# Performance work log

Measured on AMD Instinct MI355X. Metric: run time of the kernel, lower is better.

## Reference

```python
import jax, jax.numpy as jnp
import numpy as np

N, E, D = 50000, 400000, 64
L, NA, NS = 5, 4, 3            # layers, num aggregators, num scalers
ATOM_C, ATOM_V = 9, 64         # OGB-style atom feature columns / vocab
BOND_C, BOND_V = 3, 8
EPS = 1e-5
AVG_LOG = float(np.log(9.0))   # avg_d['log'] = ln(avg_degree + 1), avg_degree = 8


def setup_inputs() -> dict:
    key = jax.random.key(0)
    ks = jax.random.split(key, 8)
    x = jax.random.randint(ks[0], (N, ATOM_C), 0, ATOM_V)
    edge_index = jax.random.randint(ks[1], (2, E), 0, N)
    edge_attr = jax.random.randint(ks[2], (E, BOND_C), 0, BOND_V)
    init = lambda k, shape, fan: (jax.random.normal(k, shape, jnp.float32) / np.sqrt(fan))
    atom_emb = init(ks[3], (ATOM_C, ATOM_V, D), D)
    bond_emb = init(ks[4], (BOND_C, BOND_V, D), D)
    pre_W = init(ks[5], (L, 3 * D, D), 3 * D)                 # pretrans: Linear(3D -> D)
    pre_b = jnp.zeros((L, D), jnp.float32)
    post_W = init(ks[6], (L, (NA * NS + 1) * D, D), (NA * NS + 1) * D)  # posttrans: Linear(13D -> D)
    post_b = jnp.zeros((L, D), jnp.float32)
    return dict(x=x, edge_index=edge_index, edge_attr=edge_attr,
                atom_emb=atom_emb, bond_emb=bond_emb,
                pre_W=pre_W, pre_b=pre_b, post_W=post_W, post_b=post_b)


def reference(x, edge_index, edge_attr, atom_emb, bond_emb, pre_W, pre_b, post_W, post_b):
    src, dst = edge_index[0], edge_index[1]  # PyG: x_j = x[edge_index[0]], x_i = x[edge_index[1]]
    # Encoders: sum of per-column categorical embeddings (OGB Atom/BondEncoder)
    h0 = atom_emb[jnp.arange(ATOM_C)[None, :], x].sum(axis=1)        # [N, D]
    e = bond_emb[jnp.arange(BOND_C)[None, :], edge_attr].sum(axis=1)  # [E, D]
    # message input cat([x_i, x_j, edge_attr]) -- identical for every layer since
    # PNAGNN.forward never feeds layer output back in as x (faithful to source)
    z2 = jnp.concatenate([h0[dst], h0[src], e], axis=-1)              # [E, 3D]
    deg = jax.ops.segment_sum(jnp.ones((E,), jnp.float32), dst, num_segments=N)
    degc = jnp.maximum(deg, 1.0)[:, None]
    log_deg = jnp.log(jnp.maximum(deg, 1.0) + 1.0)[:, None]           # guard deg=0 for attenuation
    amp = log_deg / AVG_LOG
    att = AVG_LOG / log_deg
    has = (deg > 0)[:, None]
    h_in = h0
    for l in range(L):
        m = z2 @ pre_W[l] + pre_b[l]                                  # pretrans (1 layer, no act)
        s_sum = jax.ops.segment_sum(m, dst, num_segments=N)
        mean = s_sum / degc
        mx = jnp.where(has, jax.ops.segment_max(m, dst, num_segments=N), 0.0)
        mn = jnp.where(has, jax.ops.segment_min(m, dst, num_segments=N), 0.0)
        mean_sq = jax.ops.segment_sum(m * m, dst, num_segments=N) / degc
        var = jax.nn.relu(mean_sq - mean * mean)
        std = jnp.sqrt(var + EPS)
        agg = jnp.concatenate([mean, mx, mn, std], axis=-1)           # [N, 4D]
        scaled = jnp.concatenate([agg, agg * amp, agg * att], axis=-1)  # [N, 12D]
        hcat = jnp.concatenate([scaled, h0], axis=-1)                 # [N, 13D]
        out = hcat @ post_W[l] + post_b[l]                            # posttrans (1 layer, no act)
        h = out + h_in                                                # PNAGNN residual
        h_in = h
    return h
```

## Files before the change

kernel.cpp:

```cpp
#include <hip/hip_runtime.h>
#include <hip/hip_bf16.h>

#define NN 50000
#define NE 400000
#define AVG_LOG_F 2.1972245773362196f
#define EPSV 1e-5f

typedef __hip_bfloat16 bf16;
typedef __attribute__((ext_vector_type(8))) short short8v;
typedef __attribute__((ext_vector_type(4))) float f32x4;
typedef __attribute__((ext_vector_type(2))) _Float16 h2v;

__device__ __forceinline__ float b2f(bf16 v){ return __bfloat162float(v); }
__device__ __forceinline__ bf16  f2b(float v){ return __float2bfloat16(v); }
__device__ __forceinline__ short f2s(float v){
  bf16 b = __float2bfloat16(v);
  short s; __builtin_memcpy(&s, &b, 2); return s;
}
__device__ __forceinline__ float s2f(short v){
  bf16 b; __builtin_memcpy(&b, &v, 2); return __bfloat162float(b);
}

__global__ void k_h0(const int* __restrict__ x, const float* __restrict__ aemb,
                     bf16* __restrict__ h0b){
  int idx = blockIdx.x * 256 + threadIdx.x;
  if (idx >= NN * 64) return;
  int n = idx >> 6, d = idx & 63;
  float acc = 0.f;
  #pragma unroll
  for (int c = 0; c < 9; ++c){
    int a = x[n * 9 + c];
    acc += aemb[(c * 64 + a) * 64 + d];
  }
  h0b[idx] = f2b(acc);
}

__global__ void k_deg_code(const int* __restrict__ ei, const int* __restrict__ ea,
                           int* __restrict__ deg, int* __restrict__ code){
  int e = blockIdx.x * 256 + threadIdx.x;
  if (e >= NE) return;
  int dst = ei[NE + e];
  atomicAdd(&deg[dst], 1);
  code[e] = ea[e * 3] + 8 * ea[e * 3 + 1] + 64 * ea[e * 3 + 2];
}

__global__ void k_scan1(const int* __restrict__ deg, int* __restrict__ rowptr,
                        int* __restrict__ part){
  __shared__ int s[256];
  int t = threadIdx.x, i = blockIdx.x * 256 + t;
  int v = (i < NN) ? deg[i] : 0;
  s[t] = v; __syncthreads();
  for (int off = 1; off < 256; off <<= 1){
    int xv = (t >= off) ? s[t - off] : 0;
    __syncthreads();
    s[t] += xv;
    __syncthreads();
  }
  if (i < NN) rowptr[i] = s[t] - v;
  if (t == 255) part[blockIdx.x] = s[255];
}

__global__ void k_scan2(int* __restrict__ part, int nblk){
  __shared__ int s[256];
  int t = threadIdx.x;
  int v = (t < nblk) ? part[t] : 0;
  s[t] = v; __syncthreads();
  for (int off = 1; off < 256; off <<= 1){
    int xv = (t >= off) ? s[t - off] : 0;
    __syncthreads();
    s[t] += xv;
    __syncthreads();
  }
  if (t < nblk) part[t] = s[t] - v;
}

__global__ void k_scan3(int* __restrict__ rowptr, const int* __restrict__ part,
                        const int* __restrict__ deg, float* __restrict__ amp,
                        float* __restrict__ att){
  int i = blockIdx.x * 256 + threadIdx.x;
  if (i < NN){
    rowptr[i] += part[blockIdx.x];
    int d = deg[i];
    float ld = logf((float)max(d, 1) + 1.0f);
    amp[i] = ld / AVG_LOG_F;
    att[i] = AVG_LOG_F / ld;
  }
  if (i == 0) rowptr[NN] = NE;
}

__global__ void k_scatter(const int* __restrict__ ei, const int* __restrict__ code,
                          const int* __restrict__ rowptr, int* __restrict__ cursor,
                          int2* __restrict__ sedge){
  int e = blockIdx.x * 256 + threadIdx.x;
  if (e >= NE) return;
  int dst = ei[NE + e];
  int pos = rowptr[dst] + atomicAdd(&cursor[dst], 1);
  int2 v; v.x = ei[e] * 1664 + 640; v.y = code[e] * 1024;
  sedge[pos] = v;
}

__global__ void k_ctab(const float* __restrict__ bemb, const float* __restrict__ preW,
                       _Float16* __restrict__ CTp){
  __shared__ float et[64];
  int cb = blockIdx.x, l = blockIdx.y, t = threadIdx.x;
  int a0 = cb & 7, a1 = (cb >> 3) & 7, a2 = (cb >> 6) & 7;
  et[t] = bemb[(0 * 8 + a0) * 64 + t] + bemb[(1 * 8 + a1) * 64 + t] + bemb[(2 * 8 + a2) * 64 + t];
  __syncthreads();
  float acc = 0.f;
  const float* W = preW + (l * 192 + 128) * 64;
  for (int k = 0; k < 64; ++k) acc += et[k] * W[k * 64 + t];
  CTp[((size_t)cb * 64 + t) * 8 + l] = (_Float16)acc;
}

__global__ void k_whsum(const float* __restrict__ postW, const float* __restrict__ postb,
                        float* __restrict__ whs, float* __restrict__ bs){
  int idx = blockIdx.x * 256 + threadIdx.x;
  if (idx < 4096){
    int k = idx >> 6, d = idx & 63;
    float a = 0.f;
    for (int l = 0; l < 5; ++l) a += postW[(size_t)(l * 832 + 768 + k) * 64 + d];
    whs[idx] = a;
  }
  if (idx < 64){
    float a = 0.f;
    for (int l = 0; l < 5; ++l) a += postb[l * 64 + idx];
    bs[idx] = a;
  }
}

__global__ void k_wtk(const float* __restrict__ postW, bf16* __restrict__ WtKf){
  int idx = blockIdx.x * 256 + threadIdx.x;
  if (idx >= 40 * 12 * 64 * 8) return;
  int s   = idx / 6144;
  int rem = idx % 6144;
  int gw  = rem / 512;
  int lane = (rem % 512) / 8;
  int j   = idx & 7;
  int g = gw >> 2, w4 = gw & 3;
  int kp = s * 32 + (lane >> 4) * 8 + j;
  int l = kp >> 8, kl = kp & 255;
  int c = w4 * 16 + (lane & 15);
  WtKf[idx] = f2b(postW[((size_t)l * 832 + g * 256 + kl) * 64 + c]);
}

__global__ void k_wtpre896(const float* __restrict__ preW, const float* __restrict__ preb,
                           const float* __restrict__ whs, const float* __restrict__ bs,
                           bf16* __restrict__ Wtp, float* __restrict__ bias896){
  int idx = blockIdx.x * 256 + threadIdx.x;
  if (idx < 896 * 64){
    int gc = idx >> 6, k = idx & 63;
    float v;
    if (gc < 320){
      int l = gc >> 6, c = gc & 63;
      v = preW[(size_t)(l * 192 + k) * 64 + c];
    } else if (gc < 832){
      int q = gc - 320, d = q >> 3, l = q & 7;
      v = (l < 5) ? preW[(size_t)(l * 192 + 64 + k) * 64 + d] : 0.f;
    } else {
      int c = gc - 832;
      v = whs[k * 64 + c] + ((k == c) ? 1.f : 0.f);
    }
    Wtp[idx] = f2b(v);
  }
  if (idx < 896){
    float b;
    if (idx < 320)      b = preb[(idx >> 6) * 64 + (idx & 63)];
    else if (idx < 832) b = 0.f;
    else                b = bs[idx - 832];
    bias896[idx] = b;
  }
}

__global__ __launch_bounds__(256) void k_ab_mfma(const bf16* __restrict__ h0b,
                                                 const bf16* __restrict__ Wtp,
                                                 const float* __restrict__ bias896,
                                                 _Float16* __restrict__ ABU,
                                                 float* __restrict__ out){
  __shared__ bf16 As[128][72];
  __shared__ bf16 Bs[128][72];
  const int t = threadIdx.x;
  const int n0 = blockIdx.x * 128;
  const int gc0 = blockIdx.y * 128;
  const int lane = t & 63, wid = t >> 6;
  const int rw = wid * 32;
  const short* H  = (const short*)h0b;
  const short* Wp = (const short*)Wtp;

  #pragma unroll
  for (int i = 0; i < 4; ++i){
    int idx = t + i * 256;
    int r = idx >> 3, ko = (idx & 7) * 8;
    int n = n0 + r;
    short8v v = short8v{0,0,0,0,0,0,0,0};
    if (n < NN) v = *(const short8v*)(H + (size_t)n * 64 + ko);
    *(short8v*)&As[r][ko] = v;
  }
  #pragma unroll
  for (int i = 0; i < 4; ++i){
    int idx = t + i * 256;
    int cc = idx >> 3, ko = (idx & 7) * 8;
    *(short8v*)&Bs[cc][ko] = *(const short8v*)(Wp + (size_t)(gc0 + cc) * 64 + ko);
  }
  __syncthreads();

  f32x4 acc[2][8] = {};
  #pragma unroll
  for (int kk = 0; kk < 2; ++kk){
    short8v af0 = *(const short8v*)&As[rw + (lane & 15)][kk * 32 + (lane >> 4) * 8];
    short8v af1 = *(const short8v*)&As[rw + 16 + (lane & 15)][kk * 32 + (lane >> 4) * 8];
    #pragma unroll
    for (int j = 0; j < 8; ++j){
      short8v bfj = *(const short8v*)&Bs[j * 16 + (lane & 15)][kk * 32 + (lane >> 4) * 8];
      acc[0][j] = __builtin_amdgcn_mfma_f32_16x16x32_bf16(af0, bfj, acc[0][j], 0, 0, 0);
      acc[1][j] = __builtin_amdgcn_mfma_f32_16x16x32_bf16(af1, bfj, acc[1][j], 0, 0, 0);
    }
  }

  #pragma unroll
  for (int i = 0; i < 2; ++i){
    #pragma unroll
    for (int r = 0; r < 4; ++r){
      int n = n0 + rw + i * 16 + (lane >> 4) * 4 + r;
      if (n >= NN) continue;
      #pragma unroll
      for (int j = 0; j < 8; ++j){
        int gc = gc0 + j * 16 + (lane & 15);
        float v = acc[i][j][r] + bias896[gc];
        if (gc < 832) ABU[(size_t)n * 832 + gc] = (_Float16)v;
        else          out[(size_t)n * 64 + (gc - 832)] = v;
      }
    }
  }
}

__global__ __launch_bounds__(256) void k_gather(const _Float16* __restrict__ ABU,
                                                const _Float16* __restrict__ CTp,
                                                const int* __restrict__ rowptr,
                                                const int2* __restrict__ sedge,
                                                bf16* __restrict__ AGG){
  const int t = threadIdx.x, lane = t & 63, wid = t >> 6;
  const int n = blockIdx.x * 4 + wid;
  const char* ABUb = (const char*)ABU;
  const char* CTpb = (const char*)CTp;
  short* AGs = (short*)AGG;

  int r0 = rowptr[n], r1 = rowptr[n + 1];
  float s[5]  = {0.f, 0.f, 0.f, 0.f, 0.f};
  float sq[5] = {0.f, 0.f, 0.f, 0.f, 0.f};
  const _Float16 FLO = (_Float16)(-65504.f);
  const _Float16 FHI = (_Float16)( 65504.f);
  h2v mx01 = h2v{FLO, FLO}, mx23 = h2v{FLO, FLO}, mx45 = h2v{FLO, FLO};
  h2v mn01 = h2v{FHI, FHI}, mn23 = h2v{FHI, FHI}, mn45 = h2v{FHI, FHI};

  union P8 { short8v s; h2v h[4]; };
  const int lb = lane * 16;

  for (int j = r0; j < r1; j += 4){
    int rem = r1 - j;
    int2 e0 = sedge[j];
    int2 e1 = (rem > 1) ? sedge[j + 1] : e0;
    int2 e2 = (rem > 2) ? sedge[j + 2] : e0;
    int2 e3 = (rem > 3) ? sedge[j + 3] : e0;
    P8 a0, c0, a1, c1, a2, c2, a3, c3;
    a0.s = *(const short8v*)(ABUb + e0.x + lb);
    c0.s = *(const short8v*)(CTpb + e0.y + lb);
    a1.s = *(const short8v*)(ABUb + e1.x + lb);
    c1.s = *(const short8v*)(CTpb + e1.y + lb);
    a2.s = *(const short8v*)(ABUb + e2.x + lb);
    c2.s = *(const short8v*)(CTpb + e2.y + lb);
    a3.s = *(const short8v*)(ABUb + e3.x + lb);
    c3.s = *(const short8v*)(CTpb + e3.y + lb);

    #define EDGE_ACC(A, C) {                                        \
      h2v t01 = A.h[0] + C.h[0];                                    \
      h2v t23 = A.h[1] + C.h[1];                                    \
      h2v t45 = A.h[2] + C.h[2];                                    \
      mx01 = __builtin_elementwise_max(mx01, t01);                  \
      mx23 = __builtin_elementwise_max(mx23, t23);                  \
      mx45 = __builtin_elementwise_max(mx45, t45);                  \
      mn01 = __builtin_elementwise_min(mn01, t01);                  \
      mn23 = __builtin_elementwise_min(mn23, t23);                  \
      mn45 = __builtin_elementwise_min(mn45, t45);                  \
      float f0 = (float)t01[0], f1 = (float)t01[1];                 \
      float f2 = (float)t23[0], f3 = (float)t23[1];                 \
      float f4 = (float)t45[0];                                     \
      s[0] += f0; sq[0] = fmaf(f0, f0, sq[0]);                      \
      s[1] += f1; sq[1] = fmaf(f1, f1, sq[1]);                      \
      s[2] += f2; sq[2] = fmaf(f2, f2, sq[2]);                      \
      s[3] += f3; sq[3] = fmaf(f3, f3, sq[3]);                      \
      s[4] += f4; sq[4] = fmaf(f4, f4, sq[4]);                      \
    }
    EDGE_ACC(a0, c0);
    if (rem > 1) EDGE_ACC(a1, c1);
    if (rem > 2) EDGE_ACC(a2, c2);
    if (rem > 3) EDGE_ACC(a3, c3);
    #undef EDGE_ACC
  }

  float mx[5] = {(float)mx01[0], (float)mx01[1], (float)mx23[0], (float)mx23[1], (float)mx45[0]};
  float mn[5] = {(float)mn01[0], (float)mn01[1], (float)mn23[0], (float)mn23[1], (float)mn45[0]};

  int d = r1 - r0;
  float degc = (float)((d > 0) ? d : 1);
  size_t base = (size_t)n * 1280;
  #pragma unroll
  for (int l = 0; l < 5; ++l){
    float K = (float)ABU[(size_t)n * 832 + l * 64 + lane];
    float mean = ((float)d * K + s[l]) / degc;
    float MX = (d > 0) ? (K + mx[l]) : 0.f;
    float MN = (d > 0) ? (K + mn[l]) : 0.f;
    float mu = s[l] / degc;
    float var = fmaxf(sq[l] / degc - mu * mu, 0.f);
    float sd = sqrtf(var + EPSV);
    AGs[base + l * 256 + lane]       = f2s(mean);
    AGs[base + l * 256 + 64 + lane]  = f2s(MX);
    AGs[base + l * 256 + 128 + lane] = f2s(MN);
    AGs[base + l * 256 + 192 + lane] = f2s(sd);
  }
}

__global__ __launch_bounds__(256) void k_post5(const bf16* __restrict__ AGG,
                                               const bf16* __restrict__ WtKf,
                                               const float* __restrict__ amp,
                                               const float* __restrict__ att,
                                               float* __restrict__ out){
  const int t = threadIdx.x, lane = t & 63, w4 = t >> 6;
  const int rg0 = blockIdx.x * 2;
  const char* pa0 = (const char*)AGG +
      ((size_t)(rg0 * 16) + (lane & 15)) * 2560 + (lane >> 4) * 16;
  const char* pa1 = pa0 + 16 * 2560;
  const char* pb  = (const char*)WtKf + w4 * 1024 + lane * 16;

  f32x4 acc[2][3] = {};
  for (int s = 0; s < 40; ++s){
    short8v a0 = *(const short8v*)(pa0);
    short8v a1 = *(const short8v*)(pa1);
    short8v b0 = *(const short8v*)(pb);
    short8v b1 = *(const short8v*)(pb + 4096);
    short8v b2 = *(const short8v*)(pb + 8192);
    acc[0][0] = __builtin_amdgcn_mfma_f32_16x16x32_bf16(a0, b0, acc[0][0], 0, 0, 0);
    acc[0][1] = __builtin_amdgcn_mfma_f32_16x16x32_bf16(a0, b1, acc[0][1], 0, 0, 0);
    acc[0][2] = __builtin_amdgcn_mfma_f32_16x16x32_bf16(a0, b2, acc[0][2], 0, 0, 0);
    acc[1][0] = __builtin_amdgcn_mfma_f32_16x16x32_bf16(a1, b0, acc[1][0], 0, 0, 0);
    acc[1][1] = __builtin_amdgcn_mfma_f32_16x16x32_bf16(a1, b1, acc[1][1], 0, 0, 0);
    acc[1][2] = __builtin_amdgcn_mfma_f32_16x16x32_bf16(a1, b2, acc[1][2], 0, 0, 0);
    pa0 += 64; pa1 += 64; pb += 12288;
  }

  #pragma unroll
  for (int i = 0; i < 2; ++i){
    #pragma unroll
    for (int r = 0; r < 4; ++r){
      int n = (rg0 + i) * 16 + (lane >> 4) * 4 + r;
      if (n >= NN) continue;
      float am = amp[n], at = att[n];
      int c = w4 * 16 + (lane & 15);
      out[(size_t)n * 64 + c] += acc[i][0][r] + am * acc[i][1][r] + at * acc[i][2][r];
    }
  }
}

extern "C" void kernel_launch(void* const* d_in, const int* in_sizes, int n_in,
                              void* d_out, int out_size, void* d_ws, size_t ws_size,
                              hipStream_t stream){
  const int*   x     = (const int*)d_in[0];
  const int*   ei    = (const int*)d_in[1];
  const int*   ea    = (const int*)d_in[2];
  const float* aemb  = (const float*)d_in[3];
  const float* bemb  = (const float*)d_in[4];
  const float* preW  = (const float*)d_in[5];
  const float* preb  = (const float*)d_in[6];
  const float* postW = (const float*)d_in[7];
  const float* postb = (const float*)d_in[8];
  float* out = (float*)d_out;

  char* p = (char*)d_ws;
  auto alloc = [&](size_t bytes) -> char* {
    char* r = p;
    p += (bytes + 255) & ~(size_t)255;
    return r;
  };
  bf16*      h0b     = (bf16*)     alloc((size_t)NN * 64 * 2);
  _Float16*  ABU     = (_Float16*) alloc((size_t)NN * 832 * 2);
  bf16*      AGG     = (bf16*)     alloc((size_t)(NN + 16) * 1280 * 2);
  int*       deg     = (int*)      alloc((size_t)NN * 4);
  int*       rowptr  = (int*)      alloc((size_t)(NN + 1) * 4);
  int*       cursor  = (int*)      alloc((size_t)NN * 4);
  float*     amp     = (float*)    alloc((size_t)NN * 4);
  float*     att     = (float*)    alloc((size_t)NN * 4);
  int*       code    = (int*)      alloc((size_t)NE * 4);
  int2*      sedge   = (int2*)     alloc((size_t)NE * 8);
  _Float16*  CTp     = (_Float16*) alloc((size_t)512 * 64 * 8 * 2 + 64);
  float*     whs     = (float*)    alloc((size_t)64 * 64 * 4);
  float*     bs      = (float*)    alloc((size_t)64 * 4);
  int*       part    = (int*)      alloc((size_t)256 * 4);
  bf16*      WtKf    = (bf16*)     alloc((size_t)40 * 12 * 64 * 8 * 2);
  bf16*      Wtp     = (bf16*)     alloc((size_t)896 * 64 * 2);
  float*     bias896 = (float*)    alloc((size_t)896 * 4);
  if ((size_t)(p - (char*)d_ws) > ws_size) return;

  hipMemsetAsync(deg, 0, (size_t)NN * 4, stream);
  hipMemsetAsync(cursor, 0, (size_t)NN * 4, stream);

  k_h0<<<dim3((NN * 64 + 255) / 256), 256, 0, stream>>>(x, aemb, h0b);
  k_deg_code<<<dim3((NE + 255) / 256), 256, 0, stream>>>(ei, ea, deg, code);
  int nblk = (NN + 255) / 256;
  k_scan1<<<dim3(nblk), 256, 0, stream>>>(deg, rowptr, part);
  k_scan2<<<dim3(1), 256, 0, stream>>>(part, nblk);
  k_scan3<<<dim3(nblk), 256, 0, stream>>>(rowptr, part, deg, amp, att);
  k_scatter<<<dim3((NE + 255) / 256), 256, 0, stream>>>(ei, code, rowptr, cursor, sedge);
  k_ctab<<<dim3(512, 5), 64, 0, stream>>>(bemb, preW, CTp);
  k_whsum<<<dim3(16), 256, 0, stream>>>(postW, postb, whs, bs);
  k_wtk<<<dim3((40 * 12 * 64 * 8 + 255) / 256), 256, 0, stream>>>(postW, WtKf);
  k_wtpre896<<<dim3((896 * 64 + 255) / 256), 256, 0, stream>>>(preW, preb, whs, bs,
                                                               Wtp, bias896);
  k_ab_mfma<<<dim3((NN + 127) / 128, 7), 256, 0, stream>>>(h0b, Wtp, bias896, ABU, out);
  k_gather<<<dim3(NN / 4), 256, 0, stream>>>(ABU, CTp, rowptr, sedge, AGG);
  k_post5<<<dim3((3125 + 1) / 2), 256, 0, stream>>>(AGG, WtKf, amp, att, out);
}
```

Before: 310.3 us.

## Compact per-node and edge-table layouts to remove padded lanes in gather

The per-source message-part buffer and the bond-code table drop from 8 padded layer slots to 5. They are stored as a 4-wide packed chunk plus a separate 1-wide chunk, so each lane of the gather loads 8+2 bytes instead of 16 bytes per edge. The node row is reorganised to 1280 bytes, and the fifth layer's max/min is tracked in fp32. The post-GEMM loop is also manually double-buffered so the next iteration's operands load while the current MFMAs run. This cuts wasted random-gather bandwidth, at the cost of twice as many, smaller load instructions per edge.

```diff
diff --git a/kernel.cpp b/kernel.cpp
--- a/kernel.cpp
+++ b/kernel.cpp
@@ -17,8 +17,9 @@
   bf16 b = __float2bfloat16(v);
   short s; __builtin_memcpy(&s, &b, 2); return s;
 }
-__device__ __forceinline__ float s2f(short v){
-  bf16 b; __builtin_memcpy(&b, &v, 2); return __bfloat162float(b);
+__device__ __forceinline__ short f2h(float v){
+  _Float16 h = (_Float16)v;
+  short s; __builtin_memcpy(&s, &h, 2); return s;
 }
 
 __global__ void k_h0(const int* __restrict__ x, const float* __restrict__ aemb,
@@ -95,7 +96,7 @@
   if (e >= NE) return;
   int dst = ei[NE + e];
   int pos = rowptr[dst] + atomicAdd(&cursor[dst], 1);
-  int2 v; v.x = ei[e] * 1664 + 640; v.y = code[e] * 1024;
+  int2 v; v.x = ei[e] * 1280; v.y = code[e] * 640;
   sedge[pos] = v;
 }
 
@@ -109,7 +110,9 @@
   float acc = 0.f;
   const float* W = preW + (l * 192 + 128) * 64;
   for (int k = 0; k < 64; ++k) acc += et[k] * W[k * 64 + t];
-  CTp[((size_t)cb * 64 + t) * 8 + l] = (_Float16)acc;
+  char* base = (char*)CTp + (size_t)cb * 640;
+  if (l < 4) *(short*)(base + t * 8 + l * 2) = f2h(acc);
+  else       *(short*)(base + 512 + t * 2)   = f2h(acc);
 }
 
 __global__ void k_whsum(const float* __restrict__ postW, const float* __restrict__ postb,
@@ -174,7 +177,7 @@
 __global__ __launch_bounds__(256) void k_ab_mfma(const bf16* __restrict__ h0b,
                                                  const bf16* __restrict__ Wtp,
                                                  const float* __restrict__ bias896,
-                                                 _Float16* __restrict__ ABU,
+                                                 char* __restrict__ ABU,
                                                  float* __restrict__ out){
   __shared__ bf16 As[128][72];
   __shared__ bf16 Bs[128][72];
@@ -222,26 +225,36 @@
     for (int r = 0; r < 4; ++r){
       int n = n0 + rw + i * 16 + (lane >> 4) * 4 + r;
       if (n >= NN) continue;
+      char* nb = ABU + (size_t)n * 1280;
       #pragma unroll
       for (int j = 0; j < 8; ++j){
         int gc = gc0 + j * 16 + (lane & 15);
         float v = acc[i][j][r] + bias896[gc];
-        if (gc < 832) ABU[(size_t)n * 832 + gc] = (_Float16)v;
-        else          out[(size_t)n * 64 + (gc - 832)] = v;
+        if (gc < 320){
+          *(short*)(nb + gc * 2) = f2h(v);
+        } else if (gc < 832){
+          int q = gc - 320, dd = q >> 3, l = q & 7;
+          if (l < 4)       *(short*)(nb + 640 + dd * 8 + l * 2) = f2h(v);
+          else if (l == 4) *(short*)(nb + 1152 + dd * 2)        = f2h(v);
+        } else {
+          out[(size_t)n * 64 + (gc - 832)] = v;
+        }
       }
     }
   }
 }
 
-__global__ __launch_bounds__(256) void k_gather(const _Float16* __restrict__ ABU,
-                                                const _Float16* __restrict__ CTp,
+__global__ __launch_bounds__(256) void k_gather(const char* __restrict__ ABU,
+                                                const char* __restrict__ CTp,
                                                 const int* __restrict__ rowptr,
                                                 const int2* __restrict__ sedge,
                                                 bf16* __restrict__ AGG){
   const int t = threadIdx.x, lane = t & 63, wid = t >> 6;
   const int n = blockIdx.x * 4 + wid;
-  const char* ABUb = (const char*)ABU;
-  const char* CTpb = (const char*)CTp;
+  const char* AB8 = ABU + 640;
+  const char* AB2 = ABU + 1152;
+  const char* CT8 = CTp;
+  const char* CT2 = CTp + 512;
   short* AGs = (short*)AGG;
 
   int r0 = rowptr[n], r1 = rowptr[n + 1];
@@ -249,11 +262,12 @@
   float sq[5] = {0.f, 0.f, 0.f, 0.f, 0.f};
   const _Float16 FLO = (_Float16)(-65504.f);
   const _Float16 FHI = (_Float16)( 65504.f);
-  h2v mx01 = h2v{FLO, FLO}, mx23 = h2v{FLO, FLO}, mx45 = h2v{FLO, FLO};
-  h2v mn01 = h2v{FHI, FHI}, mn23 = h2v{FHI, FHI}, mn45 = h2v{FHI, FHI};
-
-  union P8 { short8v s; h2v h[4]; };
-  const int lb = lane * 16;
+  h2v mx01 = h2v{FLO, FLO}, mx23 = h2v{FLO, FLO};
+  h2v mn01 = h2v{FHI, FHI}, mn23 = h2v{FHI, FHI};
+  float mx4 = -65504.f, mn4 = 65504.f;
+
+  union U8 { uint2 u; h2v h[2]; };
+  const int l8 = lane * 8, l2 = lane * 2;
 
   for (int j = r0; j < r1; j += 4){
     int rem = r1 - j;
@@ -261,51 +275,55 @@
     int2 e1 = (rem > 1) ? sedge[j + 1] : e0;
     int2 e2 = (rem > 2) ? sedge[j + 2] : e0;
     int2 e3 = (rem > 3) ? sedge[j + 3] : e0;
-    P8 a0, c0, a1, c1, a2, c2, a3, c3;
-    a0.s = *(const short8v*)(ABUb + e0.x + lb);
-    c0.s = *(const short8v*)(CTpb + e0.y + lb);
-    a1.s = *(const short8v*)(ABUb + e1.x + lb);
-    c1.s = *(const short8v*)(CTpb + e1.y + lb);
-    a2.s = *(const short8v*)(ABUb + e2.x + lb);
-    c2.s = *(const short8v*)(CTpb + e2.y + lb);
-    a3.s = *(const short8v*)(ABUb + e3.x + lb);
-    c3.s = *(const short8v*)(CTpb + e3.y + lb);
-
-    #define EDGE_ACC(A, C) {                                        \
+    U8 a0, a1, a2, a3, c0, c1, c2, c3;
+    unsigned short b0, b1, b2, b3, d0, d1, d2, d3;
+    a0.u = *(const uint2*)(AB8 + e0.x + l8);  b0 = *(const unsigned short*)(AB2 + e0.x + l2);
+    c0.u = *(const uint2*)(CT8 + e0.y + l8);  d0 = *(const unsigned short*)(CT2 + e0.y + l2);
+    a1.u = *(const uint2*)(AB8 + e1.x + l8);  b1 = *(const unsigned short*)(AB2 + e1.x + l2);
+    c1.u = *(const uint2*)(CT8 + e1.y + l8);  d1 = *(const unsigned short*)(CT2 + e1.y + l2);
+    a2.u = *(const uint2*)(AB8 + e2.x + l8);  b2 = *(const unsigned short*)(AB2 + e2.x + l2);
+    c2.u = *(const uint2*)(CT8 + e2.y + l8);  d2 = *(const unsigned short*)(CT2 + e2.y + l2);
+    a3.u = *(const uint2*)(AB8 + e3.x + l8);  b3 = *(const unsigned short*)(AB2 + e3.x + l2);
+    c3.u = *(const uint2*)(CT8 + e3.y + l8);  d3 = *(const unsigned short*)(CT2 + e3.y + l2);
+
+    #define EDGE_ACC(A, C, BL, DL) {                                \
       h2v t01 = A.h[0] + C.h[0];                                    \
       h2v t23 = A.h[1] + C.h[1];                                    \
-      h2v t45 = A.h[2] + C.h[2];                                    \
+      _Float16 hb, hd;                                              \
+      __builtin_memcpy(&hb, &BL, 2);                                \
+      __builtin_memcpy(&hd, &DL, 2);                                \
+      float f4 = (float)(hb + hd);                                  \
       mx01 = __builtin_elementwise_max(mx01, t01);                  \
       mx23 = __builtin_elementwise_max(mx23, t23);                  \
-      mx45 = __builtin_elementwise_max(mx45, t45);                  \
       mn01 = __builtin_elementwise_min(mn01, t01);                  \
       mn23 = __builtin_elementwise_min(mn23, t23);                  \
-      mn45 = __builtin_elementwise_min(mn45, t45);                  \
+      mx4 = fmaxf(mx4, f4); mn4 = fminf(mn4, f4);                   \
       float f0 = (float)t01[0], f1 = (float)t01[1];                 \
       float f2 = (float)t23[0], f3 = (float)t23[1];                 \
-      float f4 = (float)t45[0];                                     \
       s[0] += f0; sq[0] = fmaf(f0, f0, sq[0]);                      \
       s[1] += f1; sq[1] = fmaf(f1, f1, sq[1]);                      \
       s[2] += f2; sq[2] = fmaf(f2, f2, sq[2]);                      \
       s[3] += f3; sq[3] = fmaf(f3, f3, sq[3]);                      \
       s[4] += f4; sq[4] = fmaf(f4, f4, sq[4]);                      \
     }
-    EDGE_ACC(a0, c0);
-    if (rem > 1) EDGE_ACC(a1, c1);
-    if (rem > 2) EDGE_ACC(a2, c2);
-    if (rem > 3) EDGE_ACC(a3, c3);
+    EDGE_ACC(a0, c0, b0, d0);
+    if (rem > 1) EDGE_ACC(a1, c1, b1, d1);
+    if (rem > 2) EDGE_ACC(a2, c2, b2, d2);
+    if (rem > 3) EDGE_ACC(a3, c3, b3, d3);
     #undef EDGE_ACC
   }
 
-  float mx[5] = {(float)mx01[0], (float)mx01[1], (float)mx23[0], (float)mx23[1], (float)mx45[0]};
-  float mn[5] = {(float)mn01[0], (float)mn01[1], (float)mn23[0], (float)mn23[1], (float)mn45[0]};
+  float mx[5] = {(float)mx01[0], (float)mx01[1], (float)mx23[0], (float)mx23[1], mx4};
+  float mn[5] = {(float)mn01[0], (float)mn01[1], (float)mn23[0], (float)mn23[1], mn4};
 
   int d = r1 - r0;
   float degc = (float)((d > 0) ? d : 1);
   size_t base = (size_t)n * 1280;
+  const char* nb = ABU + (size_t)n * 1280;
   #pragma unroll
   for (int l = 0; l < 5; ++l){
-    float K = (float)ABU[(size_t)n * 832 + l * 64 + lane];
+    _Float16 Kh; __builtin_memcpy(&Kh, nb + l * 128 + lane * 2, 2);
+    float K = (float)Kh;
     float mean = ((float)d * K + s[l]) / degc;
     float MX = (d > 0) ? (K + mx[l]) : 0.f;
     float MN = (d > 0) ? (K + mn[l]) : 0.f;
@@ -332,20 +350,44 @@
   const char* pb  = (const char*)WtKf + w4 * 1024 + lane * 16;
 
   f32x4 acc[2][3] = {};
-  for (int s = 0; s < 40; ++s){
-    short8v a0 = *(const short8v*)(pa0);
-    short8v a1 = *(const short8v*)(pa1);
-    short8v b0 = *(const short8v*)(pb);
-    short8v b1 = *(const short8v*)(pb + 4096);
-    short8v b2 = *(const short8v*)(pb + 8192);
-    acc[0][0] = __builtin_amdgcn_mfma_f32_16x16x32_bf16(a0, b0, acc[0][0], 0, 0, 0);
-    acc[0][1] = __builtin_amdgcn_mfma_f32_16x16x32_bf16(a0, b1, acc[0][1], 0, 0, 0);
-    acc[0][2] = __builtin_amdgcn_mfma_f32_16x16x32_bf16(a0, b2, acc[0][2], 0, 0, 0);
-    acc[1][0] = __builtin_amdgcn_mfma_f32_16x16x32_bf16(a1, b0, acc[1][0], 0, 0, 0);
-    acc[1][1] = __builtin_amdgcn_mfma_f32_16x16x32_bf16(a1, b1, acc[1][1], 0, 0, 0);
-    acc[1][2] = __builtin_amdgcn_mfma_f32_16x16x32_bf16(a1, b2, acc[1][2], 0, 0, 0);
-    pa0 += 64; pa1 += 64; pb += 12288;
-  }
+  short8v A0a, A1a, B0a, B1a, B2a, A0b, A1b, B0b, B1b, B2b;
+  A0a = *(const short8v*)pa0;
+  A1a = *(const short8v*)pa1;
+  B0a = *(const short8v*)pb;
+  B1a = *(const short8v*)(pb + 4096);
+  B2a = *(const short8v*)(pb + 8192);
+
+  #define MFMA6(A0, A1, B0, B1, B2)                                          \
+    acc[0][0] = __builtin_amdgcn_mfma_f32_16x16x32_bf16(A0, B0, acc[0][0], 0, 0, 0); \
+    acc[0][1] = __builtin_amdgcn_mfma_f32_16x16x32_bf16(A0, B1, acc[0][1], 0, 0, 0); \
+    acc[0][2] = __builtin_amdgcn_mfma_f32_16x16x32_bf16(A0, B2, acc[0][2], 0, 0, 0); \
+    acc[1][0] = __builtin_amdgcn_mfma_f32_16x16x32_bf16(A1, B0, acc[1][0], 0, 0, 0); \
+    acc[1][1] = __builtin_amdgcn_mfma_f32_16x16x32_bf16(A1, B1, acc[1][1], 0, 0, 0); \
+    acc[1][2] = __builtin_amdgcn_mfma_f32_16x16x32_bf16(A1, B2, acc[1][2], 0, 0, 0);
+
+  for (int k = 0; k < 19; ++k){
+    A0b = *(const short8v*)(pa0 + 64);
+    A1b = *(const short8v*)(pa1 + 64);
+    B0b = *(const short8v*)(pb + 12288);
+    B1b = *(const short8v*)(pb + 12288 + 4096);
+    B2b = *(const short8v*)(pb + 12288 + 8192);
+    MFMA6(A0a, A1a, B0a, B1a, B2a);
+    pa0 += 128; pa1 += 128; pb += 24576;
+    A0a = *(const short8v*)pa0;
+    A1a = *(const short8v*)pa1;
+    B0a = *(const short8v*)pb;
+    B1a = *(const short8v*)(pb + 4096);
+    B2a = *(const short8v*)(pb + 8192);
+    MFMA6(A0b, A1b, B0b, B1b, B2b);
+  }
+  A0b = *(const short8v*)(pa0 + 64);
+  A1b = *(const short8v*)(pa1 + 64);
+  B0b = *(const short8v*)(pb + 12288);
+  B1b = *(const short8v*)(pb + 12288 + 4096);
+  B2b = *(const short8v*)(pb + 12288 + 8192);
+  MFMA6(A0a, A1a, B0a, B1a, B2a);
+  MFMA6(A0b, A1b, B0b, B1b, B2b);
+  #undef MFMA6
 
   #pragma unroll
   for (int i = 0; i < 2; ++i){
@@ -381,7 +423,7 @@
     return r;
   };
   bf16*      h0b     = (bf16*)     alloc((size_t)NN * 64 * 2);
-  _Float16*  ABU     = (_Float16*) alloc((size_t)NN * 832 * 2);
+  char*      ABU     = (char*)     alloc((size_t)NN * 1280);
   bf16*      AGG     = (bf16*)     alloc((size_t)(NN + 16) * 1280 * 2);
   int*       deg     = (int*)      alloc((size_t)NN * 4);
   int*       rowptr  = (int*)      alloc((size_t)(NN + 1) * 4);
@@ -390,7 +432,7 @@
   float*     att     = (float*)    alloc((size_t)NN * 4);
   int*       code    = (int*)      alloc((size_t)NE * 4);
   int2*      sedge   = (int2*)     alloc((size_t)NE * 8);
-  _Float16*  CTp     = (_Float16*) alloc((size_t)512 * 64 * 8 * 2 + 64);
+  _Float16*  CTp     = (_Float16*) alloc((size_t)512 * 640);
   float*     whs     = (float*)    alloc((size_t)64 * 64 * 4);
   float*     bs      = (float*)    alloc((size_t)64 * 4);
   int*       part    = (int*)      alloc((size_t)256 * 4);
@@ -415,6 +457,6 @@
   k_wtpre896<<<dim3((896 * 64 + 255) / 256), 256, 0, stream>>>(preW, preb, whs, bs,
                                                                Wtp, bias896);
   k_ab_mfma<<<dim3((NN + 127) / 128, 7), 256, 0, stream>>>(h0b, Wtp, bias896, ABU, out);
-  k_gather<<<dim3(NN / 4), 256, 0, stream>>>(ABU, CTp, rowptr, sedge, AGG);
+  k_gather<<<dim3(NN / 4), 256, 0, stream>>>(ABU, (const char*)CTp, rowptr, sedge, AGG);
   k_post5<<<dim3((3125 + 1) / 2), 256, 0, stream>>>(AGG, WtKf, amp, att, out);
 }
```

After: 312.9 us. Within noise of the previous version (+0.8%).
